# Kernel optimization log

Measured on AMD Instinct MI355X. Metric: run time of the kernel, lower is better.

The kernel has to match this reference:

```python
import jax, jax.numpy as jnp
import numpy as np

N_NODES = 100000
N_EDGES = 800000
DIM_IN = 128
DIM_OUT = 256


def setup_inputs() -> dict:
    key = jax.random.key(0)
    k1, k2, k3, k4, k5 = jax.random.split(key, 5)
    x = jax.random.normal(k1, (N_NODES, DIM_IN), dtype=jnp.float32)
    edge_index = jax.random.randint(k2, (2, N_EDGES), 0, N_NODES, dtype=jnp.int64)
    deg_inv = jax.random.uniform(k3, (N_NODES,), dtype=jnp.float32)
    W = jax.random.normal(k4, (DIM_OUT, DIM_IN), dtype=jnp.float32) * (1.0 / np.sqrt(DIM_IN))
    b = jax.random.normal(k5, (DIM_OUT,), dtype=jnp.float32) * 0.01
    return {"x": x, "edge_index": edge_index, "deg_inv": deg_inv, "W": W, "b": b}


def reference(x, edge_index, deg_inv, W, b):
    src = edge_index[0]
    dst = edge_index[1]
    # gather by src, scatter-add by dst: m[dst] += x[src]
    m = jax.ops.segment_sum(x[src], dst, num_segments=N_NODES)  # [N, dim_in]
    m = m * deg_inv[:, None]  # degree normalize
    h = m @ W.T + b  # [N, dim_out]
    h = jax.nn.gelu(h, approximate=False)  # torch F.gelu default = exact erf
    # dropout is identity in eval mode
    return h
```

## Files before the change

### kernel.cpp

```cpp
#include <hip/hip_runtime.h>
#include <math.h>

#define N_NODES 100000
#define N_EDGES 800000
#define DIM_IN 128
#define DIM_OUT 256
#define NPB 64
#define CAP 64

typedef __bf16 bf16x8 __attribute__((ext_vector_type(8)));
typedef float  f32x4  __attribute__((ext_vector_type(4)));

__global__ __launch_bounds__(256) void k_prep(const float* __restrict__ x,
                                              const float* __restrict__ W,
                                              unsigned short* __restrict__ xb,
                                              unsigned short* __restrict__ Wb,
                                              int* __restrict__ cnt) {
    int i = blockIdx.x * 256 + threadIdx.x;
    const float4 v = reinterpret_cast<const float4*>(x)[i];
    unsigned short s0 = __builtin_bit_cast(unsigned short, (__bf16)v.x);
    unsigned short s1 = __builtin_bit_cast(unsigned short, (__bf16)v.y);
    unsigned short s2 = __builtin_bit_cast(unsigned short, (__bf16)v.z);
    unsigned short s3 = __builtin_bit_cast(unsigned short, (__bf16)v.w);
    uint2 o;
    o.x = (unsigned)s0 | ((unsigned)s1 << 16);
    o.y = (unsigned)s2 | ((unsigned)s3 << 16);
    reinterpret_cast<uint2*>(xb)[i] = o;
    if (i < DIM_IN * DIM_OUT) Wb[i] = __builtin_bit_cast(unsigned short, (__bf16)W[i]);
    if (i < N_NODES) cnt[i] = 0;
}

__global__ __launch_bounds__(256) void k_fillpad(const int* __restrict__ src,
                                                 const int* __restrict__ dst,
                                                 int* __restrict__ cnt,
                                                 int* __restrict__ list) {
    int e = blockIdx.x * 256 + threadIdx.x;
    int d = dst[e];
    int pos = atomicAdd(&cnt[d], 1);
    if (pos < CAP) list[(size_t)d * CAP + pos] = src[e];
}

__device__ __forceinline__ float bflo(unsigned u) {
    return __builtin_bit_cast(float, u << 16);
}
__device__ __forceinline__ float bfhi(unsigned u) {
    return __builtin_bit_cast(float, u & 0xffff0000u);
}

__global__ __launch_bounds__(256) void k_agg(const unsigned short* __restrict__ xb,
                                             const int* __restrict__ list,
                                             const int* __restrict__ cnt,
                                             const float* __restrict__ deg_inv,
                                             unsigned short* __restrict__ mb) {
    int wave = threadIdx.x >> 6;
    int lane = threadIdx.x & 63;
    int node = blockIdx.x * 4 + wave;
    int c = __builtin_amdgcn_readfirstlane(cnt[node]);
    c = c < CAP ? c : CAP;
    const int beg = node * CAP;
    const int end = beg + c;
    float a0 = 0.f, a1 = 0.f, b0 = 0.f, b1 = 0.f;
    float c0 = 0.f, c1 = 0.f, d0 = 0.f, d1 = 0.f;
    int e = beg;
    for (; e + 7 < end; e += 8) {
        int s0 = list[e],     s1 = list[e + 1], s2 = list[e + 2], s3 = list[e + 3];
        int s4 = list[e + 4], s5 = list[e + 5], s6 = list[e + 6], s7 = list[e + 7];
        unsigned u0 = reinterpret_cast<const unsigned*>(xb + (size_t)s0 * DIM_IN)[lane];
        unsigned u1 = reinterpret_cast<const unsigned*>(xb + (size_t)s1 * DIM_IN)[lane];
        unsigned u2 = reinterpret_cast<const unsigned*>(xb + (size_t)s2 * DIM_IN)[lane];
        unsigned u3 = reinterpret_cast<const unsigned*>(xb + (size_t)s3 * DIM_IN)[lane];
        unsigned u4 = reinterpret_cast<const unsigned*>(xb + (size_t)s4 * DIM_IN)[lane];
        unsigned u5 = reinterpret_cast<const unsigned*>(xb + (size_t)s5 * DIM_IN)[lane];
        unsigned u6 = reinterpret_cast<const unsigned*>(xb + (size_t)s6 * DIM_IN)[lane];
        unsigned u7 = reinterpret_cast<const unsigned*>(xb + (size_t)s7 * DIM_IN)[lane];
        a0 += bflo(u0) + bflo(u1);  a1 += bfhi(u0) + bfhi(u1);
        b0 += bflo(u2) + bflo(u3);  b1 += bfhi(u2) + bfhi(u3);
        c0 += bflo(u4) + bflo(u5);  c1 += bfhi(u4) + bfhi(u5);
        d0 += bflo(u6) + bflo(u7);  d1 += bfhi(u6) + bfhi(u7);
    }
    for (; e + 3 < end; e += 4) {
        int s0 = list[e], s1 = list[e + 1], s2 = list[e + 2], s3 = list[e + 3];
        unsigned u0 = reinterpret_cast<const unsigned*>(xb + (size_t)s0 * DIM_IN)[lane];
        unsigned u1 = reinterpret_cast<const unsigned*>(xb + (size_t)s1 * DIM_IN)[lane];
        unsigned u2 = reinterpret_cast<const unsigned*>(xb + (size_t)s2 * DIM_IN)[lane];
        unsigned u3 = reinterpret_cast<const unsigned*>(xb + (size_t)s3 * DIM_IN)[lane];
        a0 += bflo(u0) + bflo(u1);  a1 += bfhi(u0) + bfhi(u1);
        b0 += bflo(u2) + bflo(u3);  b1 += bfhi(u2) + bfhi(u3);
    }
    for (; e < end; ++e) {
        int s0 = list[e];
        unsigned u0 = reinterpret_cast<const unsigned*>(xb + (size_t)s0 * DIM_IN)[lane];
        a0 += bflo(u0);
        a1 += bfhi(u0);
    }
    float d = deg_inv[node];
    float r0 = ((a0 + b0) + (c0 + d0)) * d;
    float r1 = ((a1 + b1) + (c1 + d1)) * d;
    unsigned short q0 = __builtin_bit_cast(unsigned short, (__bf16)r0);
    unsigned short q1 = __builtin_bit_cast(unsigned short, (__bf16)r1);
    reinterpret_cast<unsigned*>(mb + (size_t)node * DIM_IN)[lane] =
        (unsigned)q0 | ((unsigned)q1 << 16);
}

__device__ __forceinline__ float gelu_f(float h) {
    float u = h * h;
    float inner = h * (0.7978845608f + 0.0356774081f * u);
    float a = __builtin_amdgcn_exp2f(-2.8853900818f * __builtin_fabsf(inner));
    float t = (1.f - a) * __builtin_amdgcn_rcpf(1.f + a);
    t = __builtin_copysignf(t, inner);
    return 0.5f * h * (1.f + t);
}

__global__ __launch_bounds__(512, 4) void k_gemm(
    const unsigned short* __restrict__ mb,
    const unsigned short* __restrict__ Wb,
    const float* __restrict__ bias,
    float* __restrict__ out)
{
    __shared__ unsigned char mtile[NPB * 256];

    const int tid  = threadIdx.x;
    const int wave = tid >> 6;
    const int lane = tid & 63;
    const int lr = lane & 15;
    const int kg = lane >> 4;
    const int o0 = wave * 32;
    const int nb0 = blockIdx.x * NPB;

#pragma unroll
    for (int p = 0; p < 2; ++p) {
        const int idx = p * 512 + tid;
        const int row = idx >> 4;
        const int g   = idx & 15;
        const uint4 v = *reinterpret_cast<const uint4*>(
            mb + (size_t)(nb0 + row) * DIM_IN + g * 8);
        const int swg = g ^ (row & 7);
        *reinterpret_cast<uint4*>(&mtile[row * 256 + swg * 16]) = v;
    }

    bf16x8 wfr[2][4];
#pragma unroll
    for (int mt = 0; mt < 2; ++mt)
#pragma unroll
        for (int ks = 0; ks < 4; ++ks)
            wfr[mt][ks] = *reinterpret_cast<const bf16x8*>(
                Wb + (size_t)(o0 + mt * 16 + lr) * DIM_IN + ks * 32 + kg * 8);

    f32x4 bias4[2];
#pragma unroll
    for (int mt = 0; mt < 2; ++mt)
        bias4[mt] = *reinterpret_cast<const f32x4*>(bias + o0 + mt * 16 + kg * 4);

    __syncthreads();

#pragma unroll
    for (int st = 0; st < NPB / 32; ++st) {
        const int nb = nb0 + st * 32;
        if (nb >= N_NODES) break;

        f32x4 acc[2][2] = {};
#pragma unroll
        for (int ks = 0; ks < 4; ++ks) {
            bf16x8 mfr[2];
#pragma unroll
            for (int nt = 0; nt < 2; ++nt) {
                const int row = st * 32 + nt * 16 + lr;
                const int g = (ks * 4 + kg) ^ (row & 7);
                mfr[nt] = *reinterpret_cast<const bf16x8*>(&mtile[row * 256 + g * 16]);
            }
#pragma unroll
            for (int mt = 0; mt < 2; ++mt)
#pragma unroll
                for (int nt = 0; nt < 2; ++nt)
                    acc[mt][nt] = __builtin_amdgcn_mfma_f32_16x16x32_bf16(
                        wfr[mt][ks], mfr[nt], acc[mt][nt], 0, 0, 0);
        }

#pragma unroll
        for (int nt = 0; nt < 2; ++nt) {
            const int node = nb + nt * 16 + lr;
            if (node < N_NODES) {
                float* orow = out + (size_t)node * DIM_OUT + o0 + kg * 4;
#pragma unroll
                for (int mt = 0; mt < 2; ++mt) {
                    f32x4 h = acc[mt][nt] + bias4[mt];
                    f32x4 g;
                    g[0] = gelu_f(h[0]);
                    g[1] = gelu_f(h[1]);
                    g[2] = gelu_f(h[2]);
                    g[3] = gelu_f(h[3]);
                    *reinterpret_cast<f32x4*>(orow + mt * 16) = g;
                }
            }
        }
    }
}

extern "C" void kernel_launch(void* const* d_in, const int* in_sizes, int n_in,
                              void* d_out, int out_size, void* d_ws, size_t ws_size,
                              hipStream_t stream) {
    const float* x       = (const float*)d_in[0];
    const int*   ei      = (const int*)d_in[1];
    const float* deg_inv = (const float*)d_in[2];
    const float* W       = (const float*)d_in[3];
    const float* bias    = (const float*)d_in[4];
    float*       out     = (float*)d_out;

    const int* src = ei;
    const int* dst = ei + N_EDGES;

    unsigned short* mb = (unsigned short*)d_ws;
    int* cnt  = (int*)(mb + (size_t)N_NODES * DIM_IN);
    int* list = cnt + N_NODES;
    unsigned short* Wb = (unsigned short*)(list + (size_t)N_NODES * CAP);
    unsigned short* xb = Wb + DIM_IN * DIM_OUT;

    k_prep   <<<(N_NODES * DIM_IN / 4) / 256, 256, 0, stream>>>(x, W, xb, Wb, cnt);
    k_fillpad<<<N_EDGES / 256, 256, 0, stream>>>(src, dst, cnt, list);
    k_agg    <<<N_NODES / 4, 256, 0, stream>>>(xb, list, cnt, deg_inv, mb);
    k_gemm   <<<(N_NODES + NPB - 1) / NPB, 512, 0, stream>>>(mb, Wb, bias, out);
}
```

Before: 139.3 us.

## Fuse neighbor aggregation into GEMM kernel via shared-memory tile

```diff
diff --git a/kernel.cpp b/kernel.cpp
--- a/kernel.cpp
+++ b/kernel.cpp
@@ -46,62 +46,6 @@
 __device__ __forceinline__ float bfhi(unsigned u) {
     return __builtin_bit_cast(float, u & 0xffff0000u);
 }
-
-__global__ __launch_bounds__(256) void k_agg(const unsigned short* __restrict__ xb,
-                                             const int* __restrict__ list,
-                                             const int* __restrict__ cnt,
-                                             const float* __restrict__ deg_inv,
-                                             unsigned short* __restrict__ mb) {
-    int wave = threadIdx.x >> 6;
-    int lane = threadIdx.x & 63;
-    int node = blockIdx.x * 4 + wave;
-    int c = __builtin_amdgcn_readfirstlane(cnt[node]);
-    c = c < CAP ? c : CAP;
-    const int beg = node * CAP;
-    const int end = beg + c;
-    float a0 = 0.f, a1 = 0.f, b0 = 0.f, b1 = 0.f;
-    float c0 = 0.f, c1 = 0.f, d0 = 0.f, d1 = 0.f;
-    int e = beg;
-    for (; e + 7 < end; e += 8) {
-        int s0 = list[e],     s1 = list[e + 1], s2 = list[e + 2], s3 = list[e + 3];
-        int s4 = list[e + 4], s5 = list[e + 5], s6 = list[e + 6], s7 = list[e + 7];
-        unsigned u0 = reinterpret_cast<const unsigned*>(xb + (size_t)s0 * DIM_IN)[lane];
-        unsigned u1 = reinterpret_cast<const unsigned*>(xb + (size_t)s1 * DIM_IN)[lane];
-        unsigned u2 = reinterpret_cast<const unsigned*>(xb + (size_t)s2 * DIM_IN)[lane];
-        unsigned u3 = reinterpret_cast<const unsigned*>(xb + (size_t)s3 * DIM_IN)[lane];
-        unsigned u4 = reinterpret_cast<const unsigned*>(xb + (size_t)s4 * DIM_IN)[lane];
-        unsigned u5 = reinterpret_cast<const unsigned*>(xb + (size_t)s5 * DIM_IN)[lane];
-        unsigned u6 = reinterpret_cast<const unsigned*>(xb + (size_t)s6 * DIM_IN)[lane];
-        unsigned u7 = reinterpret_cast<const unsigned*>(xb + (size_t)s7 * DIM_IN)[lane];
-        a0 += bflo(u0) + bflo(u1);  a1 += bfhi(u0) + bfhi(u1);
-        b0 += bflo(u2) + bflo(u3);  b1 += bfhi(u2) + bfhi(u3);
-        c0 += bflo(u4) + bflo(u5);  c1 += bfhi(u4) + bfhi(u5);
-        d0 += bflo(u6) + bflo(u7);  d1 += bfhi(u6) + bfhi(u7);
-    }
-    for (; e + 3 < end; e += 4) {
-        int s0 = list[e], s1 = list[e + 1], s2 = list[e + 2], s3 = list[e + 3];
-        unsigned u0 = reinterpret_cast<const unsigned*>(xb + (size_t)s0 * DIM_IN)[lane];
-        unsigned u1 = reinterpret_cast<const unsigned*>(xb + (size_t)s1 * DIM_IN)[lane];
-        unsigned u2 = reinterpret_cast<const unsigned*>(xb + (size_t)s2 * DIM_IN)[lane];
-        unsigned u3 = reinterpret_cast<const unsigned*>(xb + (size_t)s3 * DIM_IN)[lane];
-        a0 += bflo(u0) + bflo(u1);  a1 += bfhi(u0) + bfhi(u1);
-        b0 += bflo(u2) + bflo(u3);  b1 += bfhi(u2) + bfhi(u3);
-    }
-    for (; e < end; ++e) {
-        int s0 = list[e];
-        unsigned u0 = reinterpret_cast<const unsigned*>(xb + (size_t)s0 * DIM_IN)[lane];
-        a0 += bflo(u0);
-        a1 += bfhi(u0);
-    }
-    float d = deg_inv[node];
-    float r0 = ((a0 + b0) + (c0 + d0)) * d;
-    float r1 = ((a1 + b1) + (c1 + d1)) * d;
-    unsigned short q0 = __builtin_bit_cast(unsigned short, (__bf16)r0);
-    unsigned short q1 = __builtin_bit_cast(unsigned short, (__bf16)r1);
-    reinterpret_cast<unsigned*>(mb + (size_t)node * DIM_IN)[lane] =
-        (unsigned)q0 | ((unsigned)q1 << 16);
-}
-
 __device__ __forceinline__ float gelu_f(float h) {
     float u = h * h;
     float inner = h * (0.7978845608f + 0.0356774081f * u);
@@ -111,8 +55,11 @@
     return 0.5f * h * (1.f + t);
 }
 
-__global__ __launch_bounds__(512, 4) void k_gemm(
-    const unsigned short* __restrict__ mb,
+__global__ __launch_bounds__(512, 4) void k_aggemm(
+    const unsigned short* __restrict__ xb,
+    const int* __restrict__ list,
+    const int* __restrict__ cnt,
+    const float* __restrict__ deg_inv,
     const unsigned short* __restrict__ Wb,
     const float* __restrict__ bias,
     float* __restrict__ out)
@@ -127,16 +74,63 @@
     const int o0 = wave * 32;
     const int nb0 = blockIdx.x * NPB;
 
-#pragma unroll
-    for (int p = 0; p < 2; ++p) {
-        const int idx = p * 512 + tid;
-        const int row = idx >> 4;
-        const int g   = idx & 15;
-        const uint4 v = *reinterpret_cast<const uint4*>(
-            mb + (size_t)(nb0 + row) * DIM_IN + g * 8);
-        const int swg = g ^ (row & 7);
-        *reinterpret_cast<uint4*>(&mtile[row * 256 + swg * 16]) = v;
+    const int gw   = lane >> 2;
+    const int bofs = (lane & 3) * 4;
+#pragma unroll
+    for (int i = 0; i < 8; ++i) {
+        const int row  = wave * 8 + i;
+        const int node = nb0 + row;
+        float r0 = 0.f, r1 = 0.f;
+        if (node < N_NODES) {
+            int c = __builtin_amdgcn_readfirstlane(cnt[node]);
+            c = c < CAP ? c : CAP;
+            const int beg = node * CAP;
+            const int end = beg + c;
+            float a0 = 0.f, a1 = 0.f, b0 = 0.f, b1 = 0.f;
+            float c0 = 0.f, c1 = 0.f, d0 = 0.f, d1 = 0.f;
+            int e = beg;
+            for (; e + 7 < end; e += 8) {
+                int s0 = list[e],     s1 = list[e + 1], s2 = list[e + 2], s3 = list[e + 3];
+                int s4 = list[e + 4], s5 = list[e + 5], s6 = list[e + 6], s7 = list[e + 7];
+                unsigned u0 = reinterpret_cast<const unsigned*>(xb + (size_t)s0 * DIM_IN)[lane];
+                unsigned u1 = reinterpret_cast<const unsigned*>(xb + (size_t)s1 * DIM_IN)[lane];
+                unsigned u2 = reinterpret_cast<const unsigned*>(xb + (size_t)s2 * DIM_IN)[lane];
+                unsigned u3 = reinterpret_cast<const unsigned*>(xb + (size_t)s3 * DIM_IN)[lane];
+                unsigned u4 = reinterpret_cast<const unsigned*>(xb + (size_t)s4 * DIM_IN)[lane];
+                unsigned u5 = reinterpret_cast<const unsigned*>(xb + (size_t)s5 * DIM_IN)[lane];
+                unsigned u6 = reinterpret_cast<const unsigned*>(xb + (size_t)s6 * DIM_IN)[lane];
+                unsigned u7 = reinterpret_cast<const unsigned*>(xb + (size_t)s7 * DIM_IN)[lane];
+                a0 += bflo(u0) + bflo(u1);  a1 += bfhi(u0) + bfhi(u1);
+                b0 += bflo(u2) + bflo(u3);  b1 += bfhi(u2) + bfhi(u3);
+                c0 += bflo(u4) + bflo(u5);  c1 += bfhi(u4) + bfhi(u5);
+                d0 += bflo(u6) + bflo(u7);  d1 += bfhi(u6) + bfhi(u7);
+            }
+            for (; e + 3 < end; e += 4) {
+                int s0 = list[e], s1 = list[e + 1], s2 = list[e + 2], s3 = list[e + 3];
+                unsigned u0 = reinterpret_cast<const unsigned*>(xb + (size_t)s0 * DIM_IN)[lane];
+                unsigned u1 = reinterpret_cast<const unsigned*>(xb + (size_t)s1 * DIM_IN)[lane];
+                unsigned u2 = reinterpret_cast<const unsigned*>(xb + (size_t)s2 * DIM_IN)[lane];
+                unsigned u3 = reinterpret_cast<const unsigned*>(xb + (size_t)s3 * DIM_IN)[lane];
+                a0 += bflo(u0) + bflo(u1);  a1 += bfhi(u0) + bfhi(u1);
+                b0 += bflo(u2) + bflo(u3);  b1 += bfhi(u2) + bfhi(u3);
+            }
+            for (; e < end; ++e) {
+                int s0 = list[e];
+                unsigned u0 = reinterpret_cast<const unsigned*>(xb + (size_t)s0 * DIM_IN)[lane];
+                a0 += bflo(u0);
+                a1 += bfhi(u0);
+            }
+            float d = deg_inv[node];
+            r0 = ((a0 + b0) + (c0 + d0)) * d;
+            r1 = ((a1 + b1) + (c1 + d1)) * d;
+        }
+        unsigned short q0 = __builtin_bit_cast(unsigned short, (__bf16)r0);
+        unsigned short q1 = __builtin_bit_cast(unsigned short, (__bf16)r1);
+        unsigned packed = (unsigned)q0 | ((unsigned)q1 << 16);
+        *reinterpret_cast<unsigned*>(
+            &mtile[row * 256 + ((gw ^ (row & 7)) * 16) + bofs]) = packed;
     }
+    __syncthreads();
 
     bf16x8 wfr[2][4];
 #pragma unroll
@@ -150,8 +144,6 @@
 #pragma unroll
     for (int mt = 0; mt < 2; ++mt)
         bias4[mt] = *reinterpret_cast<const f32x4*>(bias + o0 + mt * 16 + kg * 4);
-
-    __syncthreads();
 
 #pragma unroll
     for (int st = 0; st < NPB / 32; ++st) {
@@ -209,14 +201,13 @@
     const int* src = ei;
     const int* dst = ei + N_EDGES;
 
-    unsigned short* mb = (unsigned short*)d_ws;
-    int* cnt  = (int*)(mb + (size_t)N_NODES * DIM_IN);
+    int* cnt  = (int*)d_ws;
     int* list = cnt + N_NODES;
     unsigned short* Wb = (unsigned short*)(list + (size_t)N_NODES * CAP);
     unsigned short* xb = Wb + DIM_IN * DIM_OUT;
 
     k_prep   <<<(N_NODES * DIM_IN / 4) / 256, 256, 0, stream>>>(x, W, xb, Wb, cnt);
     k_fillpad<<<N_EDGES / 256, 256, 0, stream>>>(src, dst, cnt, list);
-    k_agg    <<<N_NODES / 4, 256, 0, stream>>>(xb, list, cnt, deg_inv, mb);
-    k_gemm   <<<(N_NODES + NPB - 1) / NPB, 512, 0, stream>>>(mb, Wb, bias, out);
-}
+    k_aggemm <<<(N_NODES + NPB - 1) / NPB, 512, 0, stream>>>(xb, list, cnt, deg_inv,
+                                                             Wb, bias, out);
+}
```

Measured after the change: 165.8 us. 1.19x slower.
